# Kernel optimization log

Hardware: AMD Instinct MI355X
Metric: run time of the kernel (lower is better)

Reference implementation:

```python
import jax, jax.numpy as jnp
import numpy as np


def setup_inputs() -> dict:
    key = jax.random.key(0)
    k0, k1, k2, k3, k4 = jax.random.split(key, 5)
    B, F, E = 16384, 39, 64
    R = max(1, F // 3)  # reduction_ratio = 3 -> 13
    return {
        "inputs": jax.random.normal(k0, (B, F, E), dtype=jnp.float32),
        "W_1": jax.random.normal(k1, (F, R), dtype=jnp.float32) * (2.0 / (F + R)) ** 0.5,
        "W_2": jax.random.normal(k2, (R, F), dtype=jnp.float32) * (2.0 / (F + R)) ** 0.5,
        "W_3": jax.random.normal(k3, (F, R), dtype=jnp.float32) * (2.0 / (F + R)) ** 0.5,
        "W_4": jax.random.normal(k4, (R, F), dtype=jnp.float32) * (2.0 / (F + R)) ** 0.5,
    }


def reference(inputs, W_1, W_2, W_3, W_4):
    # inputs: [B, F, E] (fields already concatenated along axis=1)
    # --- SE-style gating branch ---
    Z = jnp.mean(inputs, axis=-1)                       # [B, F]
    A_2 = jax.nn.relu(jax.nn.relu(Z @ W_1) @ W_2)       # [B, F]
    V = inputs * A_2[:, :, None]                        # [B, F, E]
    # --- soft-threshold branch ---
    inputs_abs = jnp.abs(inputs)
    abs_mean = jnp.mean(inputs_abs, axis=-1)            # [B, F]
    A_2_ = jax.nn.relu(jax.nn.relu(abs_mean @ W_3) @ W_4)  # [B, F]
    thres = (abs_mean * A_2_)[:, :, None]               # [B, F, 1]
    n_sub = jnp.maximum(inputs_abs - thres, 0.0)        # soft threshold magnitude
    R = jnp.sign(inputs) * n_sub                        # [B, F, E]
    # concat on embedding axis; original then splits into F [B,1,2E] slices
    return jnp.concatenate([V, R], axis=-1)             # [B, F, 2E]
```

## Files before the change

kernel.cpp:

```cpp
#include <hip/hip_runtime.h>


#define SEST_B 16384
#define SEST_F 39
#define SEST_E 64
#define SEST_R 13

__global__ __launch_bounds__(256) void sest_kernel(
    const float* __restrict__ x,
    const float* __restrict__ W1,
    const float* __restrict__ W2,
    const float* __restrict__ W3,
    const float* __restrict__ W4,
    float* __restrict__ out)
{
    const int b    = blockIdx.x;
    const int tid  = threadIdx.x;
    const int w    = tid >> 6;
    const int lane = tid & 63;
    const int g    = lane >> 4;
    const int s    = lane & 15;

    __shared__ float Zm[SEST_F];
    __shared__ float Am[SEST_F];
    __shared__ float H1[SEST_R];
    __shared__ float H2[SEST_R];
    __shared__ float A2s[SEST_F];
    __shared__ float Th[SEST_F];

    const float4* in4 = reinterpret_cast<const float4*>(x)
                        + (size_t)b * SEST_F * (SEST_E / 4);

    float4 xr[3];
    #pragma unroll
    for (int i = 0; i < 3; ++i) {
        const int f = i * 16 + w * 4 + g;
        float sx = 0.f, sa = 0.f;
        if (f < SEST_F) {
            float4 v = in4[f * (SEST_E / 4) + s];
            xr[i] = v;
            sx = v.x + v.y + v.z + v.w;
            sa = fabsf(v.x) + fabsf(v.y) + fabsf(v.z) + fabsf(v.w);
        }
        #pragma unroll
        for (int m = 1; m < 16; m <<= 1) {
            sx += __shfl_xor(sx, m);
            sa += __shfl_xor(sa, m);
        }
        if (f < SEST_F && s == 0) {
            Zm[f] = sx * (1.0f / 64.0f);
            Am[f] = sa * (1.0f / 64.0f);
        }
    }
    __syncthreads();

    if (tid < SEST_R) {
        float acc = 0.f;
        #pragma unroll
        for (int f = 0; f < SEST_F; ++f) acc += Zm[f] * W1[f * SEST_R + tid];
        H1[tid] = fmaxf(acc, 0.f);
    } else if (tid >= 64 && tid < 64 + SEST_R) {
        const int r = tid - 64;
        float acc = 0.f;
        #pragma unroll
        for (int f = 0; f < SEST_F; ++f) acc += Am[f] * W3[f * SEST_R + r];
        H2[r] = fmaxf(acc, 0.f);
    }
    __syncthreads();

    if (tid < SEST_F) {
        float acc = 0.f;
        #pragma unroll
        for (int r = 0; r < SEST_R; ++r) acc += H1[r] * W2[r * SEST_F + tid];
        A2s[tid] = fmaxf(acc, 0.f);
    } else if (tid >= 64 && tid < 64 + SEST_F) {
        const int f = tid - 64;
        float acc = 0.f;
        #pragma unroll
        for (int r = 0; r < SEST_R; ++r) acc += H2[r] * W4[r * SEST_F + f];
        Th[f] = Am[f] * fmaxf(acc, 0.f);
    }
    __syncthreads();

    float4* out4 = reinterpret_cast<float4*>(out)
                   + (size_t)b * SEST_F * (2 * SEST_E / 4);
    #pragma unroll
    for (int i = 0; i < 3; ++i) {
        const int f = i * 16 + w * 4 + g;
        if (f < SEST_F) {
            const float a2 = A2s[f];
            const float th = Th[f];
            const float4 v = xr[i];
            float4 V, R;
            V.x = v.x * a2; V.y = v.y * a2; V.z = v.z * a2; V.w = v.w * a2;
            R.x = copysignf(fmaxf(fabsf(v.x) - th, 0.f), v.x);
            R.y = copysignf(fmaxf(fabsf(v.y) - th, 0.f), v.y);
            R.z = copysignf(fmaxf(fabsf(v.z) - th, 0.f), v.z);
            R.w = copysignf(fmaxf(fabsf(v.w) - th, 0.f), v.w);
            out4[f * 32 + s]      = V;
            out4[f * 32 + 16 + s] = R;
        }
    }
}

extern "C" void kernel_launch(void* const* d_in, const int* in_sizes, int n_in,
                              void* d_out, int out_size, void* d_ws, size_t ws_size,
                              hipStream_t stream) {
    const float* x  = (const float*)d_in[0];
    const float* W1 = (const float*)d_in[1];
    const float* W2 = (const float*)d_in[2];
    const float* W3 = (const float*)d_in[3];
    const float* W4 = (const float*)d_in[4];
    float* out = (float*)d_out;

    sest_kernel<<<SEST_B, 256, 0, stream>>>(x, W1, W2, W3, W4, out);
}
```

Measured before the change: 448.6 us.

## Process one batch row per wavefront in a persistent grid with shared weights

Replaces the one-block-per-row launch with 1024 blocks of four wavefronts, each wavefront looping over four rows independently. The gating weights are staged once per block in LDS, and block-wide barriers become wave-local fences. This is meant to cut per-row launch and barrier overhead and repeated weight loads. In exchange each wave holds ten float4 registers per row and does the tiny matvecs with few active lanes, and the sequential per-wave loop gives less latency hiding.

```diff
diff --git a/kernel.cpp b/kernel.cpp
--- a/kernel.cpp
+++ b/kernel.cpp
@@ -1,10 +1,17 @@
 #include <hip/hip_runtime.h>
 
 
-#define SEST_B 16384
-#define SEST_F 39
-#define SEST_E 64
-#define SEST_R 13
+#define B_TOT 16384
+#define Fdim  39
+#define Edim  64
+#define Rdim  13
+#define FR    (Fdim * Rdim)
+#define NBLK  1024
+#define WPB   4
+#define NWAVE (NBLK * WPB)
+#define BPW   (B_TOT / NWAVE)
+
+typedef float f32x4 __attribute__((ext_vector_type(4)));
 
 __global__ __launch_bounds__(256) void sest_kernel(
     const float* __restrict__ x,
@@ -14,91 +21,107 @@
     const float* __restrict__ W4,
     float* __restrict__ out)
 {
-    const int b    = blockIdx.x;
     const int tid  = threadIdx.x;
-    const int w    = tid >> 6;
+    const int wid  = tid >> 6;
     const int lane = tid & 63;
-    const int g    = lane >> 4;
-    const int s    = lane & 15;
 
-    __shared__ float Zm[SEST_F];
-    __shared__ float Am[SEST_F];
-    __shared__ float H1[SEST_R];
-    __shared__ float H2[SEST_R];
-    __shared__ float A2s[SEST_F];
-    __shared__ float Th[SEST_F];
+    __shared__ float Ws[4 * FR];
+    __shared__ float ZmS[WPB][Fdim + 1];
+    __shared__ float AmS[WPB][Fdim + 1];
+    __shared__ float H1S[WPB][Rdim + 3];
+    __shared__ float H2S[WPB][Rdim + 3];
+    __shared__ float A2S[WPB][Fdim + 1];
+    __shared__ float ThS[WPB][Fdim + 1];
 
-    const float4* in4 = reinterpret_cast<const float4*>(x)
-                        + (size_t)b * SEST_F * (SEST_E / 4);
-
-    float4 xr[3];
-    #pragma unroll
-    for (int i = 0; i < 3; ++i) {
-        const int f = i * 16 + w * 4 + g;
-        float sx = 0.f, sa = 0.f;
-        if (f < SEST_F) {
-            float4 v = in4[f * (SEST_E / 4) + s];
-            xr[i] = v;
-            sx = v.x + v.y + v.z + v.w;
-            sa = fabsf(v.x) + fabsf(v.y) + fabsf(v.z) + fabsf(v.w);
-        }
-        #pragma unroll
-        for (int m = 1; m < 16; m <<= 1) {
-            sx += __shfl_xor(sx, m);
-            sa += __shfl_xor(sa, m);
-        }
-        if (f < SEST_F && s == 0) {
-            Zm[f] = sx * (1.0f / 64.0f);
-            Am[f] = sa * (1.0f / 64.0f);
-        }
+    for (int i = tid; i < FR; i += 256) {
+        Ws[i]          = W1[i];
+        Ws[FR + i]     = W2[i];
+        Ws[2 * FR + i] = W3[i];
+        Ws[3 * FR + i] = W4[i];
     }
     __syncthreads();
 
-    if (tid < SEST_R) {
-        float acc = 0.f;
+    float* Zm = ZmS[wid];
+    float* Am = AmS[wid];
+    float* H1 = H1S[wid];
+    float* H2 = H2S[wid];
+    float* A2 = A2S[wid];
+    float* Th = ThS[wid];
+
+    const int wave = blockIdx.x * WPB + wid;
+
+    for (int bi = 0; bi < BPW; ++bi) {
+        const int b = wave + bi * NWAVE;
+        const f32x4* in4 = (const f32x4*)x + (size_t)b * (Fdim * Edim / 4);
+
+        f32x4 xr[10];
         #pragma unroll
-        for (int f = 0; f < SEST_F; ++f) acc += Zm[f] * W1[f * SEST_R + tid];
-        H1[tid] = fmaxf(acc, 0.f);
-    } else if (tid >= 64 && tid < 64 + SEST_R) {
-        const int r = tid - 64;
-        float acc = 0.f;
+        for (int it = 0; it < 10; ++it) {
+            const int j = it * 64 + lane;
+            const int f = j >> 4, s = j & 15;
+            float px = 0.f, pa = 0.f;
+            if (j < Fdim * 16) {
+                f32x4 v = in4[f * 16 + s];
+                xr[it] = v;
+                px = v.x + v.y + v.z + v.w;
+                pa = fabsf(v.x) + fabsf(v.y) + fabsf(v.z) + fabsf(v.w);
+            }
+            #pragma unroll
+            for (int m = 1; m < 16; m <<= 1) {
+                px += __shfl_xor(px, m);
+                pa += __shfl_xor(pa, m);
+            }
+            if (j < Fdim * 16 && s == 0) {
+                Zm[f] = px * (1.0f / 64.0f);
+                Am[f] = pa * (1.0f / 64.0f);
+            }
+        }
+        __threadfence_block();
+
+        if (lane < Rdim) {
+            float acc = 0.f;
+            #pragma unroll
+            for (int f = 0; f < Fdim; ++f) acc += Zm[f] * Ws[f * Rdim + lane];
+            H1[lane] = fmaxf(acc, 0.f);
+        } else if (lane >= 32 && lane < 32 + Rdim) {
+            const int r = lane - 32;
+            float acc = 0.f;
+            #pragma unroll
+            for (int f = 0; f < Fdim; ++f) acc += Am[f] * Ws[2 * FR + f * Rdim + r];
+            H2[r] = fmaxf(acc, 0.f);
+        }
+        __threadfence_block();
+
+        if (lane < Fdim) {
+            float a = 0.f, t = 0.f;
+            #pragma unroll
+            for (int r = 0; r < Rdim; ++r) {
+                a += H1[r] * Ws[FR + r * Fdim + lane];
+                t += H2[r] * Ws[3 * FR + r * Fdim + lane];
+            }
+            A2[lane] = fmaxf(a, 0.f);
+            Th[lane] = Am[lane] * fmaxf(t, 0.f);
+        }
+        __threadfence_block();
+
+        f32x4* o4 = (f32x4*)out + (size_t)b * (Fdim * 2 * Edim / 4);
         #pragma unroll
-        for (int f = 0; f < SEST_F; ++f) acc += Am[f] * W3[f * SEST_R + r];
-        H2[r] = fmaxf(acc, 0.f);
-    }
-    __syncthreads();
-
-    if (tid < SEST_F) {
-        float acc = 0.f;
-        #pragma unroll
-        for (int r = 0; r < SEST_R; ++r) acc += H1[r] * W2[r * SEST_F + tid];
-        A2s[tid] = fmaxf(acc, 0.f);
-    } else if (tid >= 64 && tid < 64 + SEST_F) {
-        const int f = tid - 64;
-        float acc = 0.f;
-        #pragma unroll
-        for (int r = 0; r < SEST_R; ++r) acc += H2[r] * W4[r * SEST_F + f];
-        Th[f] = Am[f] * fmaxf(acc, 0.f);
-    }
-    __syncthreads();
-
-    float4* out4 = reinterpret_cast<float4*>(out)
-                   + (size_t)b * SEST_F * (2 * SEST_E / 4);
-    #pragma unroll
-    for (int i = 0; i < 3; ++i) {
-        const int f = i * 16 + w * 4 + g;
-        if (f < SEST_F) {
-            const float a2 = A2s[f];
-            const float th = Th[f];
-            const float4 v = xr[i];
-            float4 V, R;
-            V.x = v.x * a2; V.y = v.y * a2; V.z = v.z * a2; V.w = v.w * a2;
-            R.x = copysignf(fmaxf(fabsf(v.x) - th, 0.f), v.x);
-            R.y = copysignf(fmaxf(fabsf(v.y) - th, 0.f), v.y);
-            R.z = copysignf(fmaxf(fabsf(v.z) - th, 0.f), v.z);
-            R.w = copysignf(fmaxf(fabsf(v.w) - th, 0.f), v.w);
-            out4[f * 32 + s]      = V;
-            out4[f * 32 + 16 + s] = R;
+        for (int it = 0; it < 10; ++it) {
+            const int j = it * 64 + lane;
+            if (j < Fdim * 16) {
+                const int f = j >> 4, s = j & 15;
+                const float a2 = A2[f];
+                const float th = Th[f];
+                const f32x4 v = xr[it];
+                f32x4 V, Rv;
+                V.x = v.x * a2; V.y = v.y * a2; V.z = v.z * a2; V.w = v.w * a2;
+                Rv.x = copysignf(fmaxf(fabsf(v.x) - th, 0.f), v.x);
+                Rv.y = copysignf(fmaxf(fabsf(v.y) - th, 0.f), v.y);
+                Rv.z = copysignf(fmaxf(fabsf(v.z) - th, 0.f), v.z);
+                Rv.w = copysignf(fmaxf(fabsf(v.w) - th, 0.f), v.w);
+                o4[f * 32 + s]      = V;
+                o4[f * 32 + 16 + s] = Rv;
+            }
         }
     }
 }
@@ -113,5 +136,5 @@
     const float* W4 = (const float*)d_in[4];
     float* out = (float*)d_out;
 
-    sest_kernel<<<SEST_B, 256, 0, stream>>>(x, W1, W2, W3, W4, out);
+    sest_kernel<<<NBLK, 256, 0, stream>>>(x, W1, W2, W3, W4, out);
 }
```

Result: slower. 468.1 us (+4.3%).
